# Performance work log

Hardware: AMD Instinct MI355X
Metric: run time of the kernel (lower is better)

## Reference

```python
import jax, jax.numpy as jnp
import numpy as np

N_NODES = 100000
N_EDGES = 1600000
IN_CH = 3
HID = 32
BN_EPS = 1e-5


def setup_inputs() -> dict:
    key = jax.random.key(0)
    k_x, k_e1, k_e2, k_w, k_b, k_p = jax.random.split(key, 6)
    x = jax.random.normal(k_x, (N_NODES, IN_CH), dtype=jnp.float32)
    src = jax.random.randint(k_e1, (N_EDGES,), 0, N_NODES)
    dst = jax.random.randint(k_e2, (N_EDGES,), 0, N_NODES)
    edge_index = jnp.stack([src, dst]).astype(jnp.int64)
    # GCNConv linear params (glorot-ish init)
    W = jax.random.normal(k_w, (IN_CH, HID), dtype=jnp.float32) / np.sqrt(IN_CH)
    b = jnp.zeros((HID,), dtype=jnp.float32)
    bn_gamma = jnp.ones((HID,), dtype=jnp.float32)
    bn_beta = jnp.zeros((HID,), dtype=jnp.float32)
    prelu_w = jnp.full((1,), 0.25, dtype=jnp.float32)  # torch PReLU default
    return {"x": x, "edge_index": edge_index, "W": W, "b": b,
            "bn_gamma": bn_gamma, "bn_beta": bn_beta, "prelu_w": prelu_w}


def reference(x, edge_index, W, b, bn_gamma, bn_beta, prelu_w):
    src, dst = edge_index[0], edge_index[1]
    n = x.shape[0]
    # --- GCNConv: sym-normalized aggregation with self-loops ---
    # degree including self loop (edge weights = 1)
    deg = 1.0 + jax.ops.segment_sum(jnp.ones_like(src, dtype=x.dtype), dst,
                                    num_segments=n)
    dinv = jax.lax.rsqrt(deg)                       # deg^{-1/2}, [N]
    h = x @ W                                       # [N, HID]
    norm = dinv[src] * dinv[dst]                    # [E]
    msg = h[src] * norm[:, None]                    # [E, HID] gather
    agg = jax.ops.segment_sum(msg, dst, num_segments=n)  # scatter-add
    agg = agg + h * (1.0 / deg)[:, None]            # self-loop term
    agg = agg + b
    # --- BatchNorm1d (training-mode batch statistics, biased var) ---
    mean = jnp.mean(agg, axis=0)
    var = jnp.mean(jnp.square(agg - mean), axis=0)
    xhat = (agg - mean) * jax.lax.rsqrt(var + BN_EPS)
    y = xhat * bn_gamma + bn_beta
    # --- PReLU (single shared slope) ---
    y = jnp.where(y >= 0, y, prelu_w[0] * y)
    # dropout(p=0.5) is identity in eval / deterministic reference
    return y
```

## Files before the change

kernel.cpp:

```cpp
#include <hip/hip_runtime.h>

#define N_NODES 100000
#define N_EDGES 1600000
#define HID 32
#define BN_EPS 1e-5f

#define BSZ   128
#define NBUCK 782
#define CAP   3072
#define NSL   256
#define EPSL  6250
#define SRC_MASK 0x1FFFFu


__global__ __launch_bounds__(1024)
void bin_kernel(const int* __restrict__ src, const int* __restrict__ dst,
                int* __restrict__ gcur, unsigned* __restrict__ ebuf) {
    __shared__ unsigned stageP[EPSL];
    __shared__ unsigned short stageB[EPSL];
    __shared__ int hist[NBUCK], curs[NBUCK], delta[NBUCK];
    __shared__ int sc[1024];
    int tid = threadIdx.x, blk = blockIdx.x;
    int e0 = blk * EPSL;

    unsigned pk[7]; int bk[7];
#pragma unroll
    for (int i = 0; i < 7; ++i) {
        int j = tid + i * 1024;
        if (j < EPSL) {
            int e = e0 + j;
            int d = dst[e];
            bk[i] = d >> 7;
            pk[i] = ((unsigned)(d & (BSZ - 1)) << 17) | (unsigned)src[e];
        } else bk[i] = -1;
    }
    for (int j = tid; j < NBUCK; j += 1024) hist[j] = 0;
    __syncthreads();
#pragma unroll
    for (int i = 0; i < 7; ++i)
        if (bk[i] >= 0) atomicAdd(&hist[bk[i]], 1);
    __syncthreads();
    if (tid < NBUCK) delta[tid] = tid * CAP + atomicAdd(&gcur[tid], hist[tid]);
    int h = (tid < NBUCK) ? hist[tid] : 0;
    sc[tid] = h;
    __syncthreads();
    for (int off = 1; off < 1024; off <<= 1) {
        int v = (tid >= off) ? sc[tid - off] : 0;
        __syncthreads();
        sc[tid] += v;
        __syncthreads();
    }
    if (tid < NBUCK) {
        int loff = sc[tid] - h;
        curs[tid] = loff;
        delta[tid] -= loff;
    }
    __syncthreads();
#pragma unroll
    for (int i = 0; i < 7; ++i)
        if (bk[i] >= 0) {
            int pos = atomicAdd(&curs[bk[i]], 1);
            stageP[pos] = pk[i];
            stageB[pos] = (unsigned short)bk[i];
        }
    __syncthreads();
    for (int j = tid; j < EPSL; j += 1024) {
        int b = stageB[j];
        ebuf[j + delta[b]] = stageP[j];
    }
}

__global__ void degxd_kernel(const unsigned* __restrict__ ebuf, const int* __restrict__ gcur,
                             const float* __restrict__ x, float4* __restrict__ xd) {
    __shared__ int h4[4][BSZ];
    int tid = threadIdx.x, b = blockIdx.x;
    int wv = tid >> 6;
    for (int j = tid; j < 4 * BSZ; j += 256) ((int*)h4)[j] = 0;
    __syncthreads();
    int cnt = gcur[b];
    int base = b * CAP;
    for (int e = tid; e < cnt; e += 256)
        atomicAdd(&h4[wv][ebuf[base + e] >> 17], 1);
    __syncthreads();
    if (tid < BSZ) {
        int n = (b << 7) + tid;
        if (n < N_NODES) {
            int deg = h4[0][tid] + h4[1][tid] + h4[2][tid] + h4[3][tid];
            float rd = rsqrtf(1.0f + (float)deg);
            xd[n] = make_float4(x[3 * n] * rd, x[3 * n + 1] * rd, x[3 * n + 2] * rd, rd);
        }
    }
}

__global__ void accum_kernel(const unsigned* __restrict__ ebuf, const int* __restrict__ gcur,
                             const float4* __restrict__ xd, float4* __restrict__ S4,
                             float* __restrict__ stats) {
    __shared__ float S[4][BSZ][3];
    __shared__ float ls[4][9];
    int tid = threadIdx.x, b = blockIdx.x;
    int wv = tid >> 6;
    for (int j = tid; j < 4 * BSZ * 3; j += 256) ((float*)S)[j] = 0.f;
    __syncthreads();
    int cnt = gcur[b];
    int base = b * CAP;
    for (int e = tid; e < cnt; e += 256) {
        unsigned p = ebuf[base + e];
        float4 v = xd[p & SRC_MASK];
        int l = (int)(p >> 17);
        atomicAdd(&S[wv][l][0], v.x);
        atomicAdd(&S[wv][l][1], v.y);
        atomicAdd(&S[wv][l][2], v.z);
    }
    __syncthreads();
    float st[9];
#pragma unroll
    for (int q = 0; q < 9; ++q) st[q] = 0.f;
    if (tid < BSZ) {
        int n = (b << 7) + tid;
        if (n < N_NODES) {
            float4 self = xd[n];
            float sx = self.x + S[0][tid][0] + S[1][tid][0] + S[2][tid][0] + S[3][tid][0];
            float sy = self.y + S[0][tid][1] + S[1][tid][1] + S[2][tid][1] + S[3][tid][1];
            float sz = self.z + S[0][tid][2] + S[1][tid][2] + S[2][tid][2] + S[3][tid][2];
            S4[n] = make_float4(sx, sy, sz, self.w);
            float ax = self.w * sx, ay = self.w * sy, az = self.w * sz;
            st[0] = ax; st[1] = ay; st[2] = az;
            st[3] = ax * ax; st[4] = ax * ay; st[5] = ax * az;
            st[6] = ay * ay; st[7] = ay * az; st[8] = az * az;
        }
    }
    for (int m = 1; m < 64; m <<= 1)
#pragma unroll
        for (int q = 0; q < 9; ++q) st[q] += __shfl_xor(st[q], m);
    if ((tid & 63) == 0)
#pragma unroll
        for (int q = 0; q < 9; ++q) ls[wv][q] = st[q];
    __syncthreads();
    if (tid < 9) {
        float s = ls[0][tid] + ls[1][tid] + ls[2][tid] + ls[3][tid];
        atomicAdd(&stats[tid], s);
    }
}

__global__ void final_out_kernel(const float4* __restrict__ S4, const float* __restrict__ stats,
                                 const float* __restrict__ W, const float* __restrict__ bb,
                                 const float* __restrict__ gamma, const float* __restrict__ beta,
                                 const float* __restrict__ prelu, float* __restrict__ out) {
    __shared__ float cb[4 * HID];
    int tid = threadIdx.x;
    if (tid < HID) {
        int c = tid;
        float m1x = stats[0], m1y = stats[1], m1z = stats[2];
        float Mxx = stats[3], Mxy = stats[4], Mxz = stats[5];
        float Myy = stats[6], Myz = stats[7], Mzz = stats[8];
        float w0 = W[c], w1 = W[HID + c], w2 = W[2 * HID + c];
        const float invn = 1.0f / (float)N_NODES;
        float m1w = m1x * w0 + m1y * w1 + m1z * w2;
        float mean = m1w * invn + bb[c];
        float quad = w0 * w0 * Mxx + w1 * w1 * Myy + w2 * w2 * Mzz
                   + 2.f * (w0 * w1 * Mxy + w0 * w2 * Mxz + w1 * w2 * Myz);
        float ex2 = quad * invn + 2.f * bb[c] * m1w * invn + bb[c] * bb[c];
        float var = ex2 - mean * mean;
        float sc = gamma[c] * rsqrtf(var + BN_EPS);
        cb[c] = w0 * sc;
        cb[HID + c] = w1 * sc;
        cb[2 * HID + c] = w2 * sc;
        cb[3 * HID + c] = bb[c] * sc + (beta[c] - mean * sc);
    }
    __syncthreads();
    float a = prelu[0];
    int stride = gridDim.x * blockDim.x;
    for (int t = blockIdx.x * blockDim.x + tid; t < N_NODES * HID; t += stride) {
        int n = t >> 5, c = t & 31;
        float4 s = S4[n];
        float y = s.w * (s.x * cb[c] + s.y * cb[HID + c] + s.z * cb[2 * HID + c])
                + cb[3 * HID + c];
        out[t] = y >= 0.f ? y : a * y;
    }
}


__global__ void fb_count_kernel(const int* __restrict__ dst, int* __restrict__ cnt) {
    int e = blockIdx.x * blockDim.x + threadIdx.x;
    if (e < N_EDGES) atomicAdd(&cnt[dst[e]], 1);
}

__global__ void fb_xd_kernel(const float* __restrict__ x, const int* __restrict__ cnt,
                             float4* __restrict__ xd, float4* __restrict__ S4) {
    int n = blockIdx.x * blockDim.x + threadIdx.x;
    if (n >= N_NODES) return;
    float rd = rsqrtf(1.0f + (float)cnt[n]);
    float4 v = make_float4(x[3 * n] * rd, x[3 * n + 1] * rd, x[3 * n + 2] * rd, rd);
    xd[n] = v;
    S4[n] = v;
}

__global__ void fb_scatter_kernel(const int* __restrict__ src, const int* __restrict__ dst,
                                  const float4* __restrict__ xd, float4* __restrict__ S4) {
    int e = blockIdx.x * blockDim.x + threadIdx.x;
    if (e >= N_EDGES) return;
    int s = src[e], d = dst[e];
    float4 v = xd[s];
    float* p = (float*)&S4[d];
    atomicAdd(p + 0, v.x);
    atomicAdd(p + 1, v.y);
    atomicAdd(p + 2, v.z);
}

__global__ void fb_stats_kernel(const float4* __restrict__ S4, float* __restrict__ stats) {
    __shared__ float ls[4][9];
    int tid = threadIdx.x;
    int n = blockIdx.x * blockDim.x + tid;
    float st[9];
#pragma unroll
    for (int q = 0; q < 9; ++q) st[q] = 0.f;
    if (n < N_NODES) {
        float4 s = S4[n];
        float ax = s.w * s.x, ay = s.w * s.y, az = s.w * s.z;
        st[0] = ax; st[1] = ay; st[2] = az;
        st[3] = ax * ax; st[4] = ax * ay; st[5] = ax * az;
        st[6] = ay * ay; st[7] = ay * az; st[8] = az * az;
    }
    for (int m = 1; m < 64; m <<= 1)
#pragma unroll
        for (int q = 0; q < 9; ++q) st[q] += __shfl_xor(st[q], m);
    int wv = tid >> 6;
    if ((tid & 63) == 0)
#pragma unroll
        for (int q = 0; q < 9; ++q) ls[wv][q] = st[q];
    __syncthreads();
    if (tid < 9) {
        float s = ls[0][tid] + ls[1][tid] + ls[2][tid] + ls[3][tid];
        atomicAdd(&stats[tid], s);
    }
}


extern "C" void kernel_launch(void* const* d_in, const int* in_sizes, int n_in,
                              void* d_out, int out_size, void* d_ws, size_t ws_size,
                              hipStream_t stream) {
    const float* x     = (const float*)d_in[0];
    const int*   ei    = (const int*)d_in[1];
    const float* W     = (const float*)d_in[2];
    const float* b     = (const float*)d_in[3];
    const float* gamma = (const float*)d_in[4];
    const float* beta  = (const float*)d_in[5];
    const float* prelu = (const float*)d_in[6];

    const int* src = ei;
    const int* dst = ei + N_EDGES;
    char* ws = (char*)d_ws;
    float* out = (float*)d_out;

    const size_t NEEDED = 12812416;

    if (ws_size >= NEEDED) {
        int*      gcur  = (int*)(ws);
        float*    stats = (float*)(ws + 3136);
        unsigned* ebuf  = (unsigned*)(ws + 3200);
        float4*   xd    = (float4*)(ws + 9612416);
        float4*   S4    = (float4*)(ws + 11212416);

        hipMemsetAsync(ws, 0, 3200, stream);
        bin_kernel<<<NSL, 1024, 0, stream>>>(src, dst, gcur, ebuf);
        degxd_kernel<<<NBUCK, 256, 0, stream>>>(ebuf, gcur, x, xd);
        accum_kernel<<<NBUCK, 256, 0, stream>>>(ebuf, gcur, xd, S4, stats);
        final_out_kernel<<<2048, 256, 0, stream>>>(S4, stats, W, b, gamma, beta, prelu, out);
    } else {
        int*    cnt   = (int*)(ws);
        float*  stats = (float*)(ws + 400000);
        float4* xd    = (float4*)(ws + 400640);
        float4* S4    = (float4*)(ws + 2000640);

        hipMemsetAsync(ws, 0, 400064, stream);
        fb_count_kernel<<<(N_EDGES + 255) / 256, 256, 0, stream>>>(dst, cnt);
        fb_xd_kernel<<<(N_NODES + 255) / 256, 256, 0, stream>>>(x, cnt, xd, S4);
        fb_scatter_kernel<<<(N_EDGES + 255) / 256, 256, 0, stream>>>(src, dst, xd, S4);
        fb_stats_kernel<<<(N_NODES + 255) / 256, 256, 0, stream>>>(S4, stats);
        final_out_kernel<<<2048, 256, 0, stream>>>(S4, stats, W, b, gamma, beta, prelu, out);
    }
}
```

Before: 136.3 us.

## Vectorize edge loads, use wave-shuffle scan, pad global counters, widen accum blocks

The binning kernel now reads src/dst as int4 with 250 slices of 6400 edges and replaces the block-wide shared-memory Hillis-Steele scan with a two-level wavefront shuffle scan. The global bucket counters are padded to a 16-int stride, and their memset grows to match, to cut atomic contention on shared cache lines. The degree and accumulation kernels move to 512 threads with 8 per-wave shared histograms and read packed edges as uint4, issuing four gathers per thread. This gives more memory-level parallelism and fewer instructions per edge, at the cost of more shared memory and register pressure per block.

```diff
diff --git a/kernel.cpp b/kernel.cpp
--- a/kernel.cpp
+++ b/kernel.cpp
@@ -8,9 +8,11 @@
 #define BSZ   128
 #define NBUCK 782
 #define CAP   3072
-#define NSL   256
-#define EPSL  6250
+#define NSL   250
+#define EPSL  6400
+#define E4PB  1600
 #define SRC_MASK 0x1FFFFu
+#define GSTRIDE 16
 
 
 __global__ __launch_bounds__(1024)
@@ -19,45 +21,64 @@
     __shared__ unsigned stageP[EPSL];
     __shared__ unsigned short stageB[EPSL];
     __shared__ int hist[NBUCK], curs[NBUCK], delta[NBUCK];
-    __shared__ int sc[1024];
+    __shared__ int wsum[16];
     int tid = threadIdx.x, blk = blockIdx.x;
-    int e0 = blk * EPSL;
-
-    unsigned pk[7]; int bk[7];
-#pragma unroll
-    for (int i = 0; i < 7; ++i) {
-        int j = tid + i * 1024;
-        if (j < EPSL) {
-            int e = e0 + j;
-            int d = dst[e];
-            bk[i] = d >> 7;
-            pk[i] = ((unsigned)(d & (BSZ - 1)) << 17) | (unsigned)src[e];
-        } else bk[i] = -1;
-    }
+    const int4* d4 = (const int4*)dst + blk * E4PB;
+    const int4* s4 = (const int4*)src + blk * E4PB;
+
+    int4 dv0, dv1, sv0, sv1;
+    bool v2 = (tid + 1024) < E4PB;
+    dv0 = d4[tid]; sv0 = s4[tid];
+    if (v2) { dv1 = d4[tid + 1024]; sv1 = s4[tid + 1024]; }
+
     for (int j = tid; j < NBUCK; j += 1024) hist[j] = 0;
     __syncthreads();
-#pragma unroll
-    for (int i = 0; i < 7; ++i)
-        if (bk[i] >= 0) atomicAdd(&hist[bk[i]], 1);
-    __syncthreads();
-    if (tid < NBUCK) delta[tid] = tid * CAP + atomicAdd(&gcur[tid], hist[tid]);
+
+    unsigned pk[8]; int bk[8];
+    {
+        int dd[8] = {dv0.x, dv0.y, dv0.z, dv0.w, dv1.x, dv1.y, dv1.z, dv1.w};
+        int ss[8] = {sv0.x, sv0.y, sv0.z, sv0.w, sv1.x, sv1.y, sv1.z, sv1.w};
+#pragma unroll
+        for (int i = 0; i < 8; ++i) {
+            if (i < 4 || v2) {
+                bk[i] = dd[i] >> 7;
+                pk[i] = ((unsigned)(dd[i] & 127) << 17) | (unsigned)ss[i];
+                atomicAdd(&hist[bk[i]], 1);
+            } else bk[i] = -1;
+        }
+    }
+    __syncthreads();
+
+    int lane = tid & 63, wv = tid >> 6;
     int h = (tid < NBUCK) ? hist[tid] : 0;
-    sc[tid] = h;
-    __syncthreads();
-    for (int off = 1; off < 1024; off <<= 1) {
-        int v = (tid >= off) ? sc[tid - off] : 0;
-        __syncthreads();
-        sc[tid] += v;
-        __syncthreads();
-    }
+    int v = h;
+#pragma unroll
+    for (int off = 1; off < 64; off <<= 1) {
+        int u = __shfl_up(v, off);
+        if (lane >= off) v += u;
+    }
+    if (lane == 63) wsum[wv] = v;
+    __syncthreads();
+    if (wv == 0) {
+        int w = (lane < 16) ? wsum[lane] : 0;
+#pragma unroll
+        for (int off = 1; off < 16; off <<= 1) {
+            int u = __shfl_up(w, off);
+            if (lane >= off) w += u;
+        }
+        if (lane < 16) wsum[lane] = w;
+    }
+    __syncthreads();
+    int incl = v + (wv ? wsum[wv - 1] : 0);
     if (tid < NBUCK) {
-        int loff = sc[tid] - h;
+        int loff = incl - h;
         curs[tid] = loff;
-        delta[tid] -= loff;
-    }
-    __syncthreads();
-#pragma unroll
-    for (int i = 0; i < 7; ++i)
+        int gb = atomicAdd(&gcur[tid * GSTRIDE], h);
+        delta[tid] = tid * CAP + gb - loff;
+    }
+    __syncthreads();
+#pragma unroll
+    for (int i = 0; i < 8; ++i)
         if (bk[i] >= 0) {
             int pos = atomicAdd(&curs[bk[i]], 1);
             stageP[pos] = pk[i];
@@ -72,20 +93,28 @@
 
 __global__ void degxd_kernel(const unsigned* __restrict__ ebuf, const int* __restrict__ gcur,
                              const float* __restrict__ x, float4* __restrict__ xd) {
-    __shared__ int h4[4][BSZ];
-    int tid = threadIdx.x, b = blockIdx.x;
-    int wv = tid >> 6;
-    for (int j = tid; j < 4 * BSZ; j += 256) ((int*)h4)[j] = 0;
-    __syncthreads();
-    int cnt = gcur[b];
-    int base = b * CAP;
-    for (int e = tid; e < cnt; e += 256)
-        atomicAdd(&h4[wv][ebuf[base + e] >> 17], 1);
+    __shared__ int h8[8][BSZ];
+    int tid = threadIdx.x, b = blockIdx.x, wv = tid >> 6;
+    for (int j = tid; j < 8 * BSZ; j += 512) ((int*)h8)[j] = 0;
+    __syncthreads();
+    int cnt = gcur[b * GSTRIDE];
+    const uint4* e4 = (const uint4*)(ebuf + (size_t)b * CAP);
+    int nt4 = (cnt + 3) >> 2;
+    for (int i = tid; i < nt4; i += 512) {
+        uint4 q = e4[i];
+        int rem = cnt - (i << 2);
+        atomicAdd(&h8[wv][q.x >> 17], 1);
+        if (rem > 1) atomicAdd(&h8[wv][q.y >> 17], 1);
+        if (rem > 2) atomicAdd(&h8[wv][q.z >> 17], 1);
+        if (rem > 3) atomicAdd(&h8[wv][q.w >> 17], 1);
+    }
     __syncthreads();
     if (tid < BSZ) {
         int n = (b << 7) + tid;
         if (n < N_NODES) {
-            int deg = h4[0][tid] + h4[1][tid] + h4[2][tid] + h4[3][tid];
+            int deg = 0;
+#pragma unroll
+            for (int k = 0; k < 8; ++k) deg += h8[k][tid];
             float rd = rsqrtf(1.0f + (float)deg);
             xd[n] = make_float4(x[3 * n] * rd, x[3 * n + 1] * rd, x[3 * n + 2] * rd, rd);
         }
@@ -95,33 +124,58 @@
 __global__ void accum_kernel(const unsigned* __restrict__ ebuf, const int* __restrict__ gcur,
                              const float4* __restrict__ xd, float4* __restrict__ S4,
                              float* __restrict__ stats) {
-    __shared__ float S[4][BSZ][3];
-    __shared__ float ls[4][9];
-    int tid = threadIdx.x, b = blockIdx.x;
-    int wv = tid >> 6;
-    for (int j = tid; j < 4 * BSZ * 3; j += 256) ((float*)S)[j] = 0.f;
-    __syncthreads();
-    int cnt = gcur[b];
-    int base = b * CAP;
-    for (int e = tid; e < cnt; e += 256) {
-        unsigned p = ebuf[base + e];
-        float4 v = xd[p & SRC_MASK];
-        int l = (int)(p >> 17);
-        atomicAdd(&S[wv][l][0], v.x);
-        atomicAdd(&S[wv][l][1], v.y);
-        atomicAdd(&S[wv][l][2], v.z);
+    __shared__ float S[8][BSZ][3];
+    __shared__ float ls[8][9];
+    int tid = threadIdx.x, b = blockIdx.x, wv = tid >> 6;
+    for (int j = tid; j < 8 * BSZ * 3; j += 512) ((float*)S)[j] = 0.f;
+    __syncthreads();
+    int cnt = gcur[b * GSTRIDE];
+    const uint4* e4 = (const uint4*)(ebuf + (size_t)b * CAP);
+    int nt4 = (cnt + 3) >> 2;
+    for (int i = tid; i < nt4; i += 512) {
+        uint4 q = e4[i];
+        int rem = cnt - (i << 2);
+        float4 v0 = xd[q.x & SRC_MASK];
+        float4 v1, v2c, v3;
+        if (rem > 1) v1 = xd[q.y & SRC_MASK];
+        if (rem > 2) v2c = xd[q.z & SRC_MASK];
+        if (rem > 3) v3 = xd[q.w & SRC_MASK];
+        int l0 = (int)(q.x >> 17);
+        atomicAdd(&S[wv][l0][0], v0.x);
+        atomicAdd(&S[wv][l0][1], v0.y);
+        atomicAdd(&S[wv][l0][2], v0.z);
+        if (rem > 1) {
+            int l = (int)(q.y >> 17);
+            atomicAdd(&S[wv][l][0], v1.x);
+            atomicAdd(&S[wv][l][1], v1.y);
+            atomicAdd(&S[wv][l][2], v1.z);
+        }
+        if (rem > 2) {
+            int l = (int)(q.z >> 17);
+            atomicAdd(&S[wv][l][0], v2c.x);
+            atomicAdd(&S[wv][l][1], v2c.y);
+            atomicAdd(&S[wv][l][2], v2c.z);
+        }
+        if (rem > 3) {
+            int l = (int)(q.w >> 17);
+            atomicAdd(&S[wv][l][0], v3.x);
+            atomicAdd(&S[wv][l][1], v3.y);
+            atomicAdd(&S[wv][l][2], v3.z);
+        }
     }
     __syncthreads();
     float st[9];
 #pragma unroll
-    for (int q = 0; q < 9; ++q) st[q] = 0.f;
+    for (int q2 = 0; q2 < 9; ++q2) st[q2] = 0.f;
     if (tid < BSZ) {
         int n = (b << 7) + tid;
         if (n < N_NODES) {
             float4 self = xd[n];
-            float sx = self.x + S[0][tid][0] + S[1][tid][0] + S[2][tid][0] + S[3][tid][0];
-            float sy = self.y + S[0][tid][1] + S[1][tid][1] + S[2][tid][1] + S[3][tid][1];
-            float sz = self.z + S[0][tid][2] + S[1][tid][2] + S[2][tid][2] + S[3][tid][2];
+            float sx = self.x, sy = self.y, sz = self.z;
+#pragma unroll
+            for (int k = 0; k < 8; ++k) {
+                sx += S[k][tid][0]; sy += S[k][tid][1]; sz += S[k][tid][2];
+            }
             S4[n] = make_float4(sx, sy, sz, self.w);
             float ax = self.w * sx, ay = self.w * sy, az = self.w * sz;
             st[0] = ax; st[1] = ay; st[2] = az;
@@ -131,13 +185,15 @@
     }
     for (int m = 1; m < 64; m <<= 1)
 #pragma unroll
-        for (int q = 0; q < 9; ++q) st[q] += __shfl_xor(st[q], m);
+        for (int q2 = 0; q2 < 9; ++q2) st[q2] += __shfl_xor(st[q2], m);
     if ((tid & 63) == 0)
 #pragma unroll
-        for (int q = 0; q < 9; ++q) ls[wv][q] = st[q];
+        for (int q2 = 0; q2 < 9; ++q2) ls[wv][q2] = st[q2];
     __syncthreads();
     if (tid < 9) {
-        float s = ls[0][tid] + ls[1][tid] + ls[2][tid] + ls[3][tid];
+        float s = 0.f;
+#pragma unroll
+        for (int w = 0; w < 8; ++w) s += ls[w][tid];
         atomicAdd(&stats[tid], s);
     }
 }
@@ -252,19 +308,19 @@
     char* ws = (char*)d_ws;
     float* out = (float*)d_out;
 
-    const size_t NEEDED = 12812416;
+    const size_t NEEDED = 12859456;
 
     if (ws_size >= NEEDED) {
         int*      gcur  = (int*)(ws);
-        float*    stats = (float*)(ws + 3136);
-        unsigned* ebuf  = (unsigned*)(ws + 3200);
-        float4*   xd    = (float4*)(ws + 9612416);
-        float4*   S4    = (float4*)(ws + 11212416);
-
-        hipMemsetAsync(ws, 0, 3200, stream);
+        float*    stats = (float*)(ws + 50176);
+        unsigned* ebuf  = (unsigned*)(ws + 50240);
+        float4*   xd    = (float4*)(ws + 9659456);
+        float4*   S4    = (float4*)(ws + 11259456);
+
+        hipMemsetAsync(ws, 0, 50240, stream);
         bin_kernel<<<NSL, 1024, 0, stream>>>(src, dst, gcur, ebuf);
-        degxd_kernel<<<NBUCK, 256, 0, stream>>>(ebuf, gcur, x, xd);
-        accum_kernel<<<NBUCK, 256, 0, stream>>>(ebuf, gcur, xd, S4, stats);
+        degxd_kernel<<<NBUCK, 512, 0, stream>>>(ebuf, gcur, x, xd);
+        accum_kernel<<<NBUCK, 512, 0, stream>>>(ebuf, gcur, xd, S4, stats);
         final_out_kernel<<<2048, 256, 0, stream>>>(S4, stats, W, b, gamma, beta, prelu, out);
     } else {
         int*    cnt   = (int*)(ws);
```

New measurement: 146.7 us. 1.08x slower.
